# Kernel tuning notes

Hardware: AMD Instinct MI355X
Metric: run time of the kernel (lower is better)

The kernel has to match this reference:

```python
import jax, jax.numpy as jnp
import numpy as np

N = 500_000      # total nodes across all graphs in batch
B = 128          # batch_size (number of graphs)
S = 128          # state_size
D = 128          # aggregated_size


def setup_inputs() -> dict:
    key = jax.random.key(0)
    k1, k2, k3, k4, k5, k6 = jax.random.split(key, 6)
    nodes = jax.random.normal(k1, (N, S), dtype=jnp.float32)
    owner_masks = jax.random.randint(k2, (B, N), 0, 2, dtype=jnp.int32)
    # Linear params (torch Linear: y = x @ W.T + b); store W as [in, out] for x @ W
    scale = 1.0 / np.sqrt(S)
    Wt = jax.random.uniform(k3, (S, D), jnp.float32, -scale, scale)
    bt = jax.random.uniform(k4, (D,), jnp.float32, -scale, scale)
    Wg = jax.random.uniform(k5, (S, D), jnp.float32, -scale, scale)
    bg = jax.random.uniform(k6, (D,), jnp.float32, -scale, scale)
    return {"nodes": nodes, "owner_masks": owner_masks,
            "Wt": Wt, "bt": bt, "Wg": Wg, "bg": bg}


def reference(nodes, owner_masks, Wt, bt, Wg, bg):
    # gates = sigmoid(nodes @ Wg + bg)   [N, D]
    gates = jax.nn.sigmoid(nodes @ Wg + bg)
    # data = nodes @ Wt + bt             [N, D]
    data = nodes @ Wt + bt
    # pooled = owner_masks.float() @ (data * gates)   [B, D]
    return owner_masks.astype(jnp.float32) @ (data * gates)
```

## Files before the change

### kernel.cpp

```cpp
#include <hip/hip_runtime.h>


#define NTOT   500000
#define NBLK   512
#define NCHUNK 15625

#define BAR_LGKM()                                              \
  do {                                                          \
    asm volatile("s_waitcnt lgkmcnt(0)" ::: "memory");          \
    __builtin_amdgcn_s_barrier();                               \
  } while (0)

typedef __attribute__((ext_vector_type(8))) unsigned short ushort8;
typedef __bf16 bf16x8 __attribute__((ext_vector_type(8)));
typedef __bf16 bf16x2 __attribute__((ext_vector_type(2)));
typedef __attribute__((ext_vector_type(4))) float f32x4;

static __device__ __forceinline__ unsigned int pkbf(float a, float b) {
  bf16x2 v;
  v[0] = (__bf16)a;
  v[1] = (__bf16)b;
  return __builtin_bit_cast(unsigned int, v);
}

static __device__ __forceinline__ unsigned int mkw(int lo, int hi) {
  return (lo ? 0x3F80u : 0u) | (hi ? 0x3F800000u : 0u);
}

template <bool ATOMIC>
__global__ __launch_bounds__(512, 4)
void agg_main(const float* __restrict__ nodes, const int* __restrict__ masks,
              const float* __restrict__ Wt, const float* __restrict__ bt,
              const float* __restrict__ Wg, const float* __restrict__ bg,
              float* __restrict__ outp) {
  __shared__ __align__(16) unsigned short nodes_s[2][32][136];
  __shared__ __align__(16) unsigned short vt_s[2][128][40];

  const int tid = threadIdx.x;
  const int lane = tid & 63;
  const int w = tid >> 6;
  const int q = lane >> 4;
  const int r = lane & 15;

  bf16x8 Wf[2][4];
  const int dslc = w * 16 + r;
  const float btr = bt[dslc];
  const float bgr = bg[dslc];
#pragma unroll
  for (int ks = 0; ks < 4; ++ks) {
    ushort8 ft, fg;
#pragma unroll
    for (int j = 0; j < 8; ++j) {
      const int k = ks * 32 + q * 8 + j;
      ft[j] = __builtin_bit_cast(unsigned short, (__bf16)Wt[k * 128 + dslc]);
      fg[j] = __builtin_bit_cast(unsigned short, (__bf16)Wg[k * 128 + dslc]);
    }
    Wf[0][ks] = __builtin_bit_cast(bf16x8, ft);
    Wf[1][ks] = __builtin_bit_cast(bf16x8, fg);
  }

  f32x4 acc[8];
  const f32x4 fzero = {0.f, 0.f, 0.f, 0.f};
#pragma unroll
  for (int j = 0; j < 8; ++j) acc[j] = fzero;

  const int bid = blockIdx.x;
  const int c0 = (int)(((long long)bid * NCHUNK) / NBLK);
  const int c1 = (int)(((long long)(bid + 1) * NCHUNK) / NBLK);
  const int n = c1 - c0;

  const unsigned moff = (unsigned)(w * 16 + r) * (unsigned)NTOT + (unsigned)(q * 8);

  float4 nfA[2], nfB[2];
  int4 mi[2];

  auto issue_nodes = [&](float4 (&nf)[2], int c) {
    const float4* p = (const float4*)nodes;
    const int base = c * 1024 + tid;
    nf[0] = p[base];
    nf[1] = p[base + 512];
  };

  auto issue_masks = [&](int c) {
    const unsigned o = moff + (unsigned)c * 32u;
    mi[0] = *(const int4*)(masks + o);
    mi[1] = *(const int4*)(masks + o + 4);
  };

  auto stage = [&](int buf, const float4 (&nf)[2]) {
#pragma unroll
    for (int it = 0; it < 2; ++it) {
      const int flat = it * 512 + tid;
      const int nrow = flat >> 5, nc4 = flat & 31;
      uint2 u;
      u.x = pkbf(nf[it].x, nf[it].y);
      u.y = pkbf(nf[it].z, nf[it].w);
      *(uint2*)&nodes_s[buf][nrow][nc4 * 4] = u;
    }
  };

  auto pool_reissue = [&](int buf, int cnext) {
    uint4 u;
    u.x = mkw(mi[0].x, mi[0].y);
    u.y = mkw(mi[0].z, mi[0].w);
    u.z = mkw(mi[1].x, mi[1].y);
    u.w = mkw(mi[1].z, mi[1].w);
    issue_masks(cnext);
    const bf16x8 af = __builtin_bit_cast(bf16x8, u);
#pragma unroll
    for (int nt = 0; nt < 8; ++nt) {
      const bf16x8 bfr = *(const bf16x8*)&vt_s[buf][nt * 16 + r][q * 8];
      acc[nt] = __builtin_amdgcn_mfma_f32_16x16x32_bf16(af, bfr, acc[nt], 0, 0, 0);
    }
  };

  auto pool_last = [&](int buf) {
    uint4 u;
    u.x = mkw(mi[0].x, mi[0].y);
    u.y = mkw(mi[0].z, mi[0].w);
    u.z = mkw(mi[1].x, mi[1].y);
    u.w = mkw(mi[1].z, mi[1].w);
    const bf16x8 af = __builtin_bit_cast(bf16x8, u);
#pragma unroll
    for (int nt = 0; nt < 8; ++nt) {
      const bf16x8 bfr = *(const bf16x8*)&vt_s[buf][nt * 16 + r][q * 8];
      acc[nt] = __builtin_amdgcn_mfma_f32_16x16x32_bf16(af, bfr, acc[nt], 0, 0, 0);
    }
  };

  auto gemm_epi = [&](int buf) {
    f32x4 aD[2], aG[2];
    aD[0] = fzero; aD[1] = fzero; aG[0] = fzero; aG[1] = fzero;
#pragma unroll
    for (int ks = 0; ks < 4; ++ks) {
      const bf16x8 a0 = *(const bf16x8*)&nodes_s[buf][r][ks * 32 + q * 8];
      const bf16x8 a1 = *(const bf16x8*)&nodes_s[buf][16 + r][ks * 32 + q * 8];
      aD[0] = __builtin_amdgcn_mfma_f32_16x16x32_bf16(a0, Wf[0][ks], aD[0], 0, 0, 0);
      aD[1] = __builtin_amdgcn_mfma_f32_16x16x32_bf16(a1, Wf[0][ks], aD[1], 0, 0, 0);
      aG[0] = __builtin_amdgcn_mfma_f32_16x16x32_bf16(a0, Wf[1][ks], aG[0], 0, 0, 0);
      aG[1] = __builtin_amdgcn_mfma_f32_16x16x32_bf16(a1, Wf[1][ks], aG[1], 0, 0, 0);
    }
#pragma unroll
    for (int mt = 0; mt < 2; ++mt) {
      float v[4];
#pragma unroll
      for (int reg = 0; reg < 4; ++reg) {
        const float x = aD[mt][reg] + btr;
        const float g = aG[mt][reg] + bgr;
        v[reg] = x * __builtin_amdgcn_rcpf(1.f + __expf(-g));
      }
      uint2 u;
      u.x = pkbf(v[0], v[1]);
      u.y = pkbf(v[2], v[3]);
      *(uint2*)&vt_s[buf][dslc][mt * 16 + q * 4] = u;
    }
  };

  int i = 0;
  auto body = [&](int buf, float4 (&nf)[2]) {
    stage(buf, nf);
    BAR_LGKM();
    const int c = c0 + i;
    if (i + 2 < n) issue_nodes(nf, c + 2);
    if (i > 0) pool_reissue(buf ^ 1, c);
    gemm_epi(buf);
    ++i;
  };

  if (n > 0) {
    issue_nodes(nfA, c0);
    if (n > 1) issue_nodes(nfB, c0 + 1);
    issue_masks(c0);
  }
  while (i < n) {
    body(0, nfA);
    if (i < n) body(1, nfB);
  }
  BAR_LGKM();
  if (n > 0) pool_last((n - 1) & 1);

#pragma unroll
  for (int nt = 0; nt < 8; ++nt)
#pragma unroll
    for (int reg = 0; reg < 4; ++reg) {
      const int b = w * 16 + q * 4 + reg;
      const int d = nt * 16 + r;
      if (ATOMIC)
        atomicAdd(&outp[b * 128 + d], acc[nt][reg]);
      else
        outp[(size_t)bid * 16384 + b * 128 + d] = acc[nt][reg];
    }
}

__global__ __launch_bounds__(256)
void agg_reduce(const float* __restrict__ part, float* __restrict__ out) {
  const int gid = blockIdx.x * 256 + threadIdx.x;
  const int i4 = gid & 4095;
  const int grp = gid >> 12;
  const float4* p = (const float4*)part + (size_t)grp * 64 * 4096 + i4;
  float4 s = {0.f, 0.f, 0.f, 0.f};
#pragma unroll 8
  for (int g = 0; g < 64; ++g) {
    const float4 v = p[(size_t)g * 4096];
    s.x += v.x; s.y += v.y; s.z += v.z; s.w += v.w;
  }
  atomicAdd(&out[i4 * 4 + 0], s.x);
  atomicAdd(&out[i4 * 4 + 1], s.y);
  atomicAdd(&out[i4 * 4 + 2], s.z);
  atomicAdd(&out[i4 * 4 + 3], s.w);
}

extern "C" void kernel_launch(void* const* d_in, const int* in_sizes, int n_in,
                              void* d_out, int out_size, void* d_ws, size_t ws_size,
                              hipStream_t stream) {
  const float* nodes = (const float*)d_in[0];
  const int*   masks = (const int*)d_in[1];
  const float* Wt    = (const float*)d_in[2];
  const float* bt    = (const float*)d_in[3];
  const float* Wg    = (const float*)d_in[4];
  const float* bg    = (const float*)d_in[5];
  float* out = (float*)d_out;

  hipMemsetAsync(d_out, 0, (size_t)out_size * sizeof(float), stream);

  const size_t need = (size_t)NBLK * 16384 * sizeof(float);
  if (ws_size >= need) {
    agg_main<false><<<NBLK, 512, 0, stream>>>(nodes, masks, Wt, bt, Wg, bg, (float*)d_ws);
    agg_reduce<<<128, 256, 0, stream>>>((const float*)d_ws, out);
  } else {
    agg_main<true><<<NBLK, 512, 0, stream>>>(nodes, masks, Wt, bt, Wg, bg, out);
  }
}
```

Baseline: 535.6 us.

## Stream node tiles straight into swizzled fp32 LDS with a triple buffer

Node tiles are no longer loaded into registers, converted to bf16 and written to LDS. They are copied straight from global memory into a triple-buffered fp32 LDS area with global_load_lds, using an XOR swizzle, and converted to bf16 when each MFMA A-fragment is read. The aim is to cut the register staging and conversion stores on the load path and to keep more loads in flight through a three-deep prefetch. The cost is a much larger LDS footprint (48KB of fp32 node buffers), which may reduce the number of resident blocks per CU. The conversion work moves into the fragment reads, and correctness relies on in-order vmcnt retirement because the main loop has no explicit vmcnt wait.

Result: slower. 546.8 us (+2.1%).

```diff
diff --git a/kernel.cpp b/kernel.cpp
--- a/kernel.cpp
+++ b/kernel.cpp
@@ -4,17 +4,22 @@
 #define NTOT   500000
 #define NBLK   512
 #define NCHUNK 15625
+
+typedef __attribute__((ext_vector_type(8))) unsigned short ushort8;
+typedef __bf16 bf16x8 __attribute__((ext_vector_type(8)));
+typedef __bf16 bf16x2 __attribute__((ext_vector_type(2)));
+typedef __attribute__((ext_vector_type(4))) float f32x4;
+
+#define GLOAD16(gp, lp)                                                     \
+  __builtin_amdgcn_global_load_lds(                                         \
+      (const __attribute__((address_space(1))) void*)(gp),                  \
+      (__attribute__((address_space(3))) void*)(lp), 16, 0, 0)
 
 #define BAR_LGKM()                                              \
   do {                                                          \
     asm volatile("s_waitcnt lgkmcnt(0)" ::: "memory");          \
     __builtin_amdgcn_s_barrier();                               \
   } while (0)
-
-typedef __attribute__((ext_vector_type(8))) unsigned short ushort8;
-typedef __bf16 bf16x8 __attribute__((ext_vector_type(8)));
-typedef __bf16 bf16x2 __attribute__((ext_vector_type(2)));
-typedef __attribute__((ext_vector_type(4))) float f32x4;
 
 static __device__ __forceinline__ unsigned int pkbf(float a, float b) {
   bf16x2 v;
@@ -33,7 +38,7 @@
               const float* __restrict__ Wt, const float* __restrict__ bt,
               const float* __restrict__ Wg, const float* __restrict__ bg,
               float* __restrict__ outp) {
-  __shared__ __align__(16) unsigned short nodes_s[2][32][136];
+  __shared__ __align__(16) float nodes_f[3 * 4096];
   __shared__ __align__(16) unsigned short vt_s[2][128][40];
 
   const int tid = threadIdx.x;
@@ -70,15 +75,17 @@
   const int n = c1 - c0;
 
   const unsigned moff = (unsigned)(w * 16 + r) * (unsigned)NTOT + (unsigned)(q * 8);
-
-  float4 nfA[2], nfB[2];
   int4 mi[2];
 
-  auto issue_nodes = [&](float4 (&nf)[2], int c) {
-    const float4* p = (const float4*)nodes;
-    const int base = c * 1024 + tid;
-    nf[0] = p[base];
-    nf[1] = p[base + 512];
+  const int row0 = (w * 2 + 0) * 2 + (lane >> 5);
+  const int row1 = (w * 2 + 1) * 2 + (lane >> 5);
+  const unsigned tb0 = (unsigned)(row0 * 512 + (((lane & 31) ^ (row0 & 7)) << 4));
+  const unsigned tb1 = (unsigned)(row1 * 512 + (((lane & 31) ^ (row1 & 7)) << 4));
+
+  auto issue_gload = [&](unsigned fbase, int c) {
+    const char* gp = (const char*)nodes + (size_t)c * 16384u;
+    GLOAD16(gp + tb0, &nodes_f[fbase + (unsigned)(w * 2 + 0) * 256u]);
+    GLOAD16(gp + tb1, &nodes_f[fbase + (unsigned)(w * 2 + 1) * 256u]);
   };
 
   auto issue_masks = [&](int c) {
@@ -87,19 +94,23 @@
     mi[1] = *(const int4*)(masks + o + 4);
   };
 
-  auto stage = [&](int buf, const float4 (&nf)[2]) {
-#pragma unroll
-    for (int it = 0; it < 2; ++it) {
-      const int flat = it * 512 + tid;
-      const int nrow = flat >> 5, nc4 = flat & 31;
-      uint2 u;
-      u.x = pkbf(nf[it].x, nf[it].y);
-      u.y = pkbf(nf[it].z, nf[it].w);
-      *(uint2*)&nodes_s[buf][nrow][nc4 * 4] = u;
-    }
-  };
-
-  auto pool_reissue = [&](int buf, int cnext) {
+  auto frag = [&](unsigned fbase, int rowbase, int ks) -> bf16x8 {
+    const int row = rowbase + r;
+    const int s7 = r & 7;
+    const int lb0 = ks * 8 + q * 2;
+    const f32x4 v0 = *(const f32x4*)&nodes_f[fbase + (unsigned)(row * 128) +
+                                             (unsigned)(((lb0 + 0) ^ s7) << 2)];
+    const f32x4 v1 = *(const f32x4*)&nodes_f[fbase + (unsigned)(row * 128) +
+                                             (unsigned)(((lb0 + 1) ^ s7) << 2)];
+    uint4 u;
+    u.x = pkbf(v0[0], v0[1]);
+    u.y = pkbf(v0[2], v0[3]);
+    u.z = pkbf(v1[0], v1[1]);
+    u.w = pkbf(v1[2], v1[3]);
+    return __builtin_bit_cast(bf16x8, u);
+  };
+
+  auto pool_reissue = [&](int vbuf, int cnext) {
     uint4 u;
     u.x = mkw(mi[0].x, mi[0].y);
     u.y = mkw(mi[0].z, mi[0].w);
@@ -109,12 +120,12 @@
     const bf16x8 af = __builtin_bit_cast(bf16x8, u);
 #pragma unroll
     for (int nt = 0; nt < 8; ++nt) {
-      const bf16x8 bfr = *(const bf16x8*)&vt_s[buf][nt * 16 + r][q * 8];
+      const bf16x8 bfr = *(const bf16x8*)&vt_s[vbuf][nt * 16 + r][q * 8];
       acc[nt] = __builtin_amdgcn_mfma_f32_16x16x32_bf16(af, bfr, acc[nt], 0, 0, 0);
     }
   };
 
-  auto pool_last = [&](int buf) {
+  auto pool_last = [&](int vbuf) {
     uint4 u;
     u.x = mkw(mi[0].x, mi[0].y);
     u.y = mkw(mi[0].z, mi[0].w);
@@ -123,18 +134,18 @@
     const bf16x8 af = __builtin_bit_cast(bf16x8, u);
 #pragma unroll
     for (int nt = 0; nt < 8; ++nt) {
-      const bf16x8 bfr = *(const bf16x8*)&vt_s[buf][nt * 16 + r][q * 8];
+      const bf16x8 bfr = *(const bf16x8*)&vt_s[vbuf][nt * 16 + r][q * 8];
       acc[nt] = __builtin_amdgcn_mfma_f32_16x16x32_bf16(af, bfr, acc[nt], 0, 0, 0);
     }
   };
 
-  auto gemm_epi = [&](int buf) {
+  auto gemm_epi = [&](unsigned fbase, int vbuf) {
     f32x4 aD[2], aG[2];
     aD[0] = fzero; aD[1] = fzero; aG[0] = fzero; aG[1] = fzero;
 #pragma unroll
     for (int ks = 0; ks < 4; ++ks) {
-      const bf16x8 a0 = *(const bf16x8*)&nodes_s[buf][r][ks * 32 + q * 8];
-      const bf16x8 a1 = *(const bf16x8*)&nodes_s[buf][16 + r][ks * 32 + q * 8];
+      const bf16x8 a0 = frag(fbase, 0, ks);
+      const bf16x8 a1 = frag(fbase, 16, ks);
       aD[0] = __builtin_amdgcn_mfma_f32_16x16x32_bf16(a0, Wf[0][ks], aD[0], 0, 0, 0);
       aD[1] = __builtin_amdgcn_mfma_f32_16x16x32_bf16(a1, Wf[0][ks], aD[1], 0, 0, 0);
       aG[0] = __builtin_amdgcn_mfma_f32_16x16x32_bf16(a0, Wf[1][ks], aG[0], 0, 0, 0);
@@ -152,32 +163,40 @@
       uint2 u;
       u.x = pkbf(v[0], v[1]);
       u.y = pkbf(v[2], v[3]);
-      *(uint2*)&vt_s[buf][dslc][mt * 16 + q * 4] = u;
-    }
-  };
-
-  int i = 0;
-  auto body = [&](int buf, float4 (&nf)[2]) {
-    stage(buf, nf);
-    BAR_LGKM();
-    const int c = c0 + i;
-    if (i + 2 < n) issue_nodes(nf, c + 2);
-    if (i > 0) pool_reissue(buf ^ 1, c);
-    gemm_epi(buf);
-    ++i;
-  };
-
-  if (n > 0) {
-    issue_nodes(nfA, c0);
-    if (n > 1) issue_nodes(nfB, c0 + 1);
-    issue_masks(c0);
-  }
-  while (i < n) {
-    body(0, nfA);
-    if (i < n) body(1, nfB);
-  }
+      *(uint2*)&vt_s[vbuf][dslc][mt * 16 + q * 4] = u;
+    }
+  };
+
+  unsigned cur = 0, nxt = 4096, nx2 = 8192;
+  int vb = 0;
+
+  issue_gload(cur, c0);
+  issue_gload(nxt, n > 1 ? c0 + 1 : c0);
+  issue_masks(c0);
+  asm volatile("s_waitcnt vmcnt(4)" ::: "memory");
+  __builtin_amdgcn_s_barrier();
+
+  if (2 < n) issue_gload(nx2, c0 + 2);
+  gemm_epi(cur, 0);
+  if (n > 1) {
+    if (n > 2) asm volatile("s_waitcnt vmcnt(4) lgkmcnt(0)" ::: "memory");
+    else       asm volatile("s_waitcnt vmcnt(2) lgkmcnt(0)" ::: "memory");
+    __builtin_amdgcn_s_barrier();
+  }
+  { unsigned t = cur; cur = nxt; nxt = nx2; nx2 = t; }
+  vb = 1;
+
+  for (int i = 1; i < n; ++i) {
+    if (i + 2 < n) issue_gload(nx2, c0 + i + 2);
+    pool_reissue(vb ^ 1, c0 + i);
+    gemm_epi(cur, vb);
+    if (i + 1 < n) BAR_LGKM();
+    { unsigned t = cur; cur = nxt; nxt = nx2; nx2 = t; }
+    vb ^= 1;
+  }
+
   BAR_LGKM();
-  if (n > 0) pool_last((n - 1) & 1);
+  pool_last((n - 1) & 1);
 
 #pragma unroll
   for (int nt = 0; nt < 8; ++nt)
```
